# Kernel optimization log

Measured on AMD Instinct MI355X. Metric: run time of the kernel, lower is better.

The kernel has to match this reference:

```python
import jax, jax.numpy as jnp
import numpy as np

B, LQ, LP, D, H = 4, 512, 512, 512, 128


def setup_inputs() -> dict:
    key = jax.random.key(0)
    ks = jax.random.split(key, 5)
    hq = jax.random.normal(ks[0], (B, LQ, D), jnp.float32)
    hp = jax.random.normal(ks[1], (B, LP, D), jnp.float32)
    mask_hq = jnp.ones((B, LQ), dtype=bool)
    mask_hp = jnp.ones((B, LP), dtype=bool)
    # ln: Linear(2*D -> H) split into the hq / hp halves (algebraically identical
    # to concatenating then applying one Linear). Xavier-ish init scale.
    sc = 1.0 / np.sqrt(2 * D)
    Wq = jax.random.normal(ks[2], (D, H), jnp.float32) * sc
    Wp = jax.random.normal(ks[3], (D, H), jnp.float32) * sc
    b = jnp.zeros((H,), jnp.float32)
    v = jax.random.normal(ks[4], (H,), jnp.float32) / np.sqrt(H)
    return {"hq": hq, "hp": hp, "mask_hq": mask_hq, "mask_hp": mask_hp,
            "Wq": Wq, "Wp": Wp, "b": b, "v": v}


def reference(hq, hp, mask_hq, mask_hp, Wq, Wp, b, v):
    # ln(cat([hq_mat, hp_mat], -1)) == hq@Wq + hp@Wp + b  (decomposed, same math)
    pq = hq @ Wq                                  # (B, Lq, H)
    pp = hp @ Wp                                  # (B, Lp, H)
    h = jnp.tanh(pq[:, :, None, :] + pp[:, None, :, :] + b)   # (B, Lq, Lp, H)
    s = jnp.einsum('bqph,h->bqp', h, v)           # additive score (B, Lq, Lp)
    mask = mask_hq[:, :, None] & mask_hp[:, None, :]
    s = s - jnp.where(mask, 0.0, 10000.0).astype(s.dtype)
    a = jax.nn.softmax(s, axis=1)                 # softmax over Lq
    # q = sum_q a[b,q,p] * hq[b,q,:]  -> (B, Lp, D); dropout is identity (eval)
    return jnp.einsum('bqp,bqd->bpd', a, hq)
```

## Files before the change

### kernel.cpp

```cpp
#include <hip/hip_runtime.h>


#define NB 4
#define NLQ 512
#define NLP 512
#define ND 512
#define NH 128

#define KP 4
#define KSTRIDE ((size_t)2048 * NH)

#define SCL   2.8853900817779268f
#define LOG2E 1.4426950408889634f

typedef __attribute__((ext_vector_type(8))) short short8;
typedef __attribute__((ext_vector_type(4))) float f32x4;

__device__ __forceinline__ unsigned f2bf(float x) {
    unsigned u = __float_as_uint(x);
    return (u + 0x7FFFu + ((u >> 16) & 1u)) >> 16;
}
__device__ __forceinline__ float bf2f(unsigned h) { return __uint_as_float(h << 16); }

__global__ __launch_bounds__(256) void prep_kernel(
    const float* __restrict__ hq, const float* __restrict__ hp,
    const float* __restrict__ Wq, const float* __restrict__ Wp,
    unsigned short* __restrict__ Xh, unsigned short* __restrict__ Xl,
    unsigned short* __restrict__ WTh, unsigned short* __restrict__ WTl)
{
    __shared__ __align__(16) float wlds[128][132];
    const int bid = blockIdx.x, t = threadIdx.x;

    if (bid < 1024) {
        const int side = bid >> 9;
        const size_t base = (size_t)(bid & 511) * 2048 + (size_t)t * 8;
        const float* src = (side ? hp : hq) + base;
        float4 x0 = *reinterpret_cast<const float4*>(src);
        float4 x1 = *reinterpret_cast<const float4*>(src + 4);
        float v[8] = {x0.x,x0.y,x0.z,x0.w,x1.x,x1.y,x1.z,x1.w};
        unsigned uh[4], ul[4];
        #pragma unroll
        for (int j = 0; j < 4; ++j) {
            float a = v[2*j], c = v[2*j+1];
            unsigned ha = f2bf(a), hc = f2bf(c);
            unsigned la = f2bf(a - bf2f(ha)), lc = f2bf(c - bf2f(hc));
            uh[j] = ha | (hc << 16); ul[j] = la | (lc << 16);
        }
        unsigned short* dh = Xh + (size_t)side * 1048576 + base;
        unsigned short* dl = Xl + (size_t)side * 1048576 + base;
        *reinterpret_cast<uint4*>(dh) = make_uint4(uh[0],uh[1],uh[2],uh[3]);
        *reinterpret_cast<uint4*>(dl) = make_uint4(ul[0],ul[1],ul[2],ul[3]);
    } else {
        const int wb = bid - 1024;
        const int side = wb >> 2;
        const int k0 = (wb & 3) * 128;
        const float* W = side ? Wp : Wq;
        #pragma unroll
        for (int i = 0; i < 16; ++i) {
            int idx = t + i * 256;
            int r = idx >> 5, c4 = (idx & 31) * 4;
            *reinterpret_cast<float4*>(&wlds[r][c4]) =
                *reinterpret_cast<const float4*>(W + (size_t)(k0 + r) * NH + c4);
        }
        __syncthreads();
        const int h = t >> 1, seg = t & 1;
        unsigned short* dh = WTh + (size_t)side * 65536 + (size_t)h * 512 + k0 + seg * 64;
        unsigned short* dl = WTl + (size_t)side * 65536 + (size_t)h * 512 + k0 + seg * 64;
        for (int j = 0; j < 64; j += 4) {
            unsigned hh[4], ll[4];
            #pragma unroll
            for (int jj = 0; jj < 4; ++jj) {
                float w = wlds[seg * 64 + j + jj][h] * SCL;
                unsigned hb = f2bf(w);
                hh[jj] = hb; ll[jj] = f2bf(w - bf2f(hb));
            }
            *reinterpret_cast<uint2*>(dh + j) = make_uint2(hh[0]|(hh[1]<<16), hh[2]|(hh[3]<<16));
            *reinterpret_cast<uint2*>(dl + j) = make_uint2(ll[0]|(ll[1]<<16), ll[2]|(ll[3]<<16));
        }
    }
}

__global__ __launch_bounds__(256, 2) void proj_mfma_kernel(
    const unsigned short* __restrict__ Xh, const unsigned short* __restrict__ Xl,
    const unsigned short* __restrict__ WTh, const unsigned short* __restrict__ WTl,
    const float* __restrict__ bias,
    float* __restrict__ pqpart, float* __restrict__ pppart)
{
    __shared__ __align__(16) unsigned short XhL[32][40], XlL[32][40];
    __shared__ __align__(16) unsigned short WhL[128][40], WlL[128][40];

    const int row0 = blockIdx.x * 32;
    const int kk   = blockIdx.y;
    const int side = blockIdx.z;
    const int k0   = kk * 128;
    const int t = threadIdx.x;
    const int w = t >> 6, l = t & 63;
    const int rbase = 16 * (w & 1), hbase = 64 * (w >> 1);

    const unsigned short* xh = Xh + (size_t)side * 1048576;
    const unsigned short* xl = Xl + (size_t)side * 1048576;
    const unsigned short* wh = WTh + (size_t)side * 65536;
    const unsigned short* wl = WTl + (size_t)side * 65536;
    float* P = (side ? pppart : pqpart) + (size_t)kk * KSTRIDE;

    const int xr = t >> 3, xc = (t & 7) * 4;
    const int whh = t & 127, wseg = (t >> 7) * 16;

    f32x4 acc[4] = {};
    uint2 rxh, rxl; uint4 rwh0, rwh1, rwl0, rwl1;

    {   const size_t xo = (size_t)(row0 + xr) * 512 + k0 + xc;
        const size_t wo = (size_t)whh * 512 + k0 + wseg;
        rxh  = *reinterpret_cast<const uint2*>(xh + xo);
        rxl  = *reinterpret_cast<const uint2*>(xl + xo);
        rwh0 = *reinterpret_cast<const uint4*>(wh + wo);
        rwh1 = *reinterpret_cast<const uint4*>(wh + wo + 8);
        rwl0 = *reinterpret_cast<const uint4*>(wl + wo);
        rwl1 = *reinterpret_cast<const uint4*>(wl + wo + 8); }

    for (int st = 0; st < 4; ++st) {
        *reinterpret_cast<uint2*>(&XhL[xr][xc]) = rxh;
        *reinterpret_cast<uint2*>(&XlL[xr][xc]) = rxl;
        *reinterpret_cast<uint4*>(&WhL[whh][wseg])     = rwh0;
        *reinterpret_cast<uint4*>(&WhL[whh][wseg + 8]) = rwh1;
        *reinterpret_cast<uint4*>(&WlL[whh][wseg])     = rwl0;
        *reinterpret_cast<uint4*>(&WlL[whh][wseg + 8]) = rwl1;
        __syncthreads();
        if (st < 3) {
            const size_t xo = (size_t)(row0 + xr) * 512 + k0 + (st + 1) * 32 + xc;
            const size_t wo = (size_t)whh * 512 + k0 + (st + 1) * 32 + wseg;
            rxh  = *reinterpret_cast<const uint2*>(xh + xo);
            rxl  = *reinterpret_cast<const uint2*>(xl + xo);
            rwh0 = *reinterpret_cast<const uint4*>(wh + wo);
            rwh1 = *reinterpret_cast<const uint4*>(wh + wo + 8);
            rwl0 = *reinterpret_cast<const uint4*>(wl + wo);
            rwl1 = *reinterpret_cast<const uint4*>(wl + wo + 8);
        }
        short8 Ah = *reinterpret_cast<const short8*>(&XhL[rbase + (l & 15)][(l >> 4) * 8]);
        short8 Al = *reinterpret_cast<const short8*>(&XlL[rbase + (l & 15)][(l >> 4) * 8]);
        #pragma unroll
        for (int c = 0; c < 4; ++c) {
            short8 Bh = *reinterpret_cast<const short8*>(&WhL[hbase + c*16 + (l & 15)][(l >> 4) * 8]);
            short8 Bl = *reinterpret_cast<const short8*>(&WlL[hbase + c*16 + (l & 15)][(l >> 4) * 8]);
            acc[c] = __builtin_amdgcn_mfma_f32_16x16x32_bf16(Ah, Bh, acc[c], 0, 0, 0);
            acc[c] = __builtin_amdgcn_mfma_f32_16x16x32_bf16(Al, Bh, acc[c], 0, 0, 0);
            acc[c] = __builtin_amdgcn_mfma_f32_16x16x32_bf16(Ah, Bl, acc[c], 0, 0, 0);
        }
        __syncthreads();
    }

    const int orow = row0 + rbase + 4 * (l >> 4);
    #pragma unroll
    for (int c = 0; c < 4; ++c) {
        const int h = hbase + c * 16 + (l & 15);
        const float badd = (side == 0 && kk == 0) ? SCL * bias[h] : 0.f;
        #pragma unroll
        for (int i = 0; i < 4; ++i)
            P[(size_t)(orow + i) * NH + h] = acc[c][i] + badd;
    }
}

__global__ __launch_bounds__(256, 2) void scores_kernel(
    const float* __restrict__ pqpart,
    const float* __restrict__ pppart,
    const float* __restrict__ vvec,
    unsigned short* __restrict__ ebf,
    float* __restrict__ dsumpart)
{
    __shared__ float qT[NH][67];
    __shared__ float pT[NH][35];
    __shared__ __align__(16) float vL[NH];
    __shared__ float vsum_lds;

    const int qt = blockIdx.x * 64;
    const int pt = blockIdx.y * 32;
    const int b  = blockIdx.z;
    const int t  = threadIdx.x;

    {
        const float* src = pqpart + ((size_t)b * NLQ + qt) * NH;
        #pragma unroll
        for (int k = 0; k < 8; ++k) {
            int f4 = t + k * 256;
            int r = f4 >> 5, c = (f4 & 31) * 4;
            const float* p0 = src + (size_t)r * NH + c;
            float4 a  = *reinterpret_cast<const float4*>(p0);
            float4 b1 = *reinterpret_cast<const float4*>(p0 + KSTRIDE);
            float4 c1 = *reinterpret_cast<const float4*>(p0 + 2 * KSTRIDE);
            float4 d1 = *reinterpret_cast<const float4*>(p0 + 3 * KSTRIDE);
            qT[c + 0][r] = __builtin_amdgcn_exp2f(a.x + b1.x + c1.x + d1.x);
            qT[c + 1][r] = __builtin_amdgcn_exp2f(a.y + b1.y + c1.y + d1.y);
            qT[c + 2][r] = __builtin_amdgcn_exp2f(a.z + b1.z + c1.z + d1.z);
            qT[c + 3][r] = __builtin_amdgcn_exp2f(a.w + b1.w + c1.w + d1.w);
        }
        const float* src2 = pppart + ((size_t)b * NLP + pt) * NH;
        #pragma unroll
        for (int k = 0; k < 4; ++k) {
            int f4 = t + k * 256;
            int r = f4 >> 5, c = (f4 & 31) * 4;
            const float* p0 = src2 + (size_t)r * NH + c;
            float4 a  = *reinterpret_cast<const float4*>(p0);
            float4 b1 = *reinterpret_cast<const float4*>(p0 + KSTRIDE);
            float4 c1 = *reinterpret_cast<const float4*>(p0 + 2 * KSTRIDE);
            float4 d1 = *reinterpret_cast<const float4*>(p0 + 3 * KSTRIDE);
            pT[c + 0][r] = __builtin_amdgcn_exp2f(a.x + b1.x + c1.x + d1.x);
            pT[c + 1][r] = __builtin_amdgcn_exp2f(a.y + b1.y + c1.y + d1.y);
            pT[c + 2][r] = __builtin_amdgcn_exp2f(a.z + b1.z + c1.z + d1.z);
            pT[c + 3][r] = __builtin_amdgcn_exp2f(a.w + b1.w + c1.w + d1.w);
        }
        if (t < 32) *reinterpret_cast<float4*>(&vL[t * 4]) =
            *reinterpret_cast<const float4*>(vvec + t * 4);
    }
    __syncthreads();
    if (t < 64) {
        float s = vL[t] + vL[t + 64];
        #pragma unroll
        for (int off = 32; off; off >>= 1) s += __shfl_xor(s, off, 64);
        if (t == 0) vsum_lds = s * LOG2E;
    }
    __syncthreads();

    const int iq = t & 15;
    const int ip = t >> 4;

    float acc[4][2] = {};

    #pragma unroll 2
    for (int h = 0; h < NH; ++h) {
        float4 eq = *reinterpret_cast<const float4*>(&qT[h][4 * iq]);
        float2 ep = *reinterpret_cast<const float2*>(&pT[h][2 * ip]);
        float vh = vL[h];
        #pragma unroll
        for (int p = 0; p < 2; ++p) {
            float e  = p ? ep.y : ep.x;
            float za = fmaf(eq.x, e, 1.f), zb = fmaf(eq.y, e, 1.f);
            float zc = fmaf(eq.z, e, 1.f), zd = fmaf(eq.w, e, 1.f);
            float r1 = __builtin_amdgcn_rcpf(za * zb);
            float r2 = __builtin_amdgcn_rcpf(zc * zd);
            float v1 = vh * r1, v2 = vh * r2;
            acc[0][p] = fmaf(v1, zb, acc[0][p]);
            acc[1][p] = fmaf(v1, za, acc[1][p]);
            acc[2][p] = fmaf(v2, zd, acc[2][p]);
            acc[3][p] = fmaf(v2, zc, acc[3][p]);
        }
    }

    const float vs = vsum_lds;
    unsigned short* eo = ebf + ((size_t)b * NLP + pt + 2 * ip) * NLQ + qt + 4 * iq;
    float psum[2];
    #pragma unroll
    for (int p = 0; p < 2; ++p) {
        unsigned bb[4];
        float s = 0.f;
        #pragma unroll
        for (int j = 0; j < 4; ++j) {
            float e = __builtin_amdgcn_exp2f(fmaf(-SCL, acc[j][p], vs));
            bb[j] = f2bf(e);
            s += bf2f(bb[j]);
        }
        *reinterpret_cast<uint2*>(eo + (size_t)p * NLQ) =
            make_uint2(bb[0] | (bb[1] << 16), bb[2] | (bb[3] << 16));
        psum[p] = s;
    }
    #pragma unroll
    for (int off = 1; off < 16; off <<= 1) {
        psum[0] += __shfl_xor(psum[0], off, 64);
        psum[1] += __shfl_xor(psum[1], off, 64);
    }
    if ((t & 15) == 0) {
        dsumpart[((size_t)b * NLP + pt + 2 * ip + 0) * 8 + blockIdx.x] = psum[0];
        dsumpart[((size_t)b * NLP + pt + 2 * ip + 1) * 8 + blockIdx.x] = psum[1];
    }
}

__global__ __launch_bounds__(256, 2) void out_mfma_kernel(
    const unsigned short* __restrict__ ebf,
    const unsigned short* __restrict__ Xh,
    const unsigned short* __restrict__ Xl,
    const float* __restrict__ dsumpart,
    float* __restrict__ out)
{
    __shared__ __align__(16) unsigned short Ab[2][32][40];
    __shared__ __align__(16) unsigned short Hh[2][64][40];
    __shared__ __align__(16) unsigned short Hl[2][64][40];
    __shared__ float dsinv[32];

    const int pt = blockIdx.x;
    const int dt = blockIdx.y;
    const int bb = blockIdx.z;
    const int t  = threadIdx.x;
    const int w  = t >> 6, l = t & 63;
    const int poff = 16 * (w & 1), doff = 32 * (w >> 1);

    if (t < 32) {
        const float* dp = dsumpart + ((size_t)bb * NLP + pt * 32 + t) * 8;
        float s = 0.f;
        #pragma unroll
        for (int m = 0; m < 8; ++m) s += dp[m];
        dsinv[t] = 1.f / s;
    }

    const int ap = t >> 3, aq = (t & 7) * 4;
    const int hd = t & 63;
    const unsigned short* eb  = ebf + ((size_t)bb * NLP + pt * 32 + ap) * NLQ + aq;
    const unsigned short* hbh = Xh + ((size_t)bb * NLQ + 8 * w) * ND + dt * 64 + hd;
    const unsigned short* hbl = Xl + ((size_t)bb * NLQ + 8 * w) * ND + dt * 64 + hd;

    uint2 areg;
    unsigned shh[8], shl[8];

    areg = *reinterpret_cast<const uint2*>(eb);
    #pragma unroll
    for (int j = 0; j < 8; ++j) { shh[j] = hbh[(size_t)j * ND]; shl[j] = hbl[(size_t)j * ND]; }
    *reinterpret_cast<uint2*>(&Ab[0][ap][aq]) = areg;
    #pragma unroll
    for (int k = 0; k < 4; ++k) {
        *reinterpret_cast<unsigned*>(&Hh[0][hd][8*w + 2*k]) = shh[2*k] | (shh[2*k+1] << 16);
        *reinterpret_cast<unsigned*>(&Hl[0][hd][8*w + 2*k]) = shl[2*k] | (shl[2*k+1] << 16);
    }

    f32x4 acc0 = {0.f,0.f,0.f,0.f}, acc1 = {0.f,0.f,0.f,0.f};

    for (int st = 0; st < 16; ++st) {
        __syncthreads();
        const int cur = st & 1, nxt = cur ^ 1;
        if (st < 15) {
            areg = *reinterpret_cast<const uint2*>(eb + (st + 1) * 32);
            #pragma unroll
            for (int j = 0; j < 8; ++j) {
                shh[j] = hbh[((size_t)(st + 1) * 32 + j) * ND];
                shl[j] = hbl[((size_t)(st + 1) * 32 + j) * ND];
            }
        }
        short8 af  = *reinterpret_cast<const short8*>(&Ab[cur][poff + (l & 15)][(l >> 4) * 8]);
        short8 bh0 = *reinterpret_cast<const short8*>(&Hh[cur][doff +      (l & 15)][(l >> 4) * 8]);
        short8 bl0 = *reinterpret_cast<const short8*>(&Hl[cur][doff +      (l & 15)][(l >> 4) * 8]);
        short8 bh1 = *reinterpret_cast<const short8*>(&Hh[cur][doff + 16 + (l & 15)][(l >> 4) * 8]);
        short8 bl1 = *reinterpret_cast<const short8*>(&Hl[cur][doff + 16 + (l & 15)][(l >> 4) * 8]);
        acc0 = __builtin_amdgcn_mfma_f32_16x16x32_bf16(af, bh0, acc0, 0, 0, 0);
        acc0 = __builtin_amdgcn_mfma_f32_16x16x32_bf16(af, bl0, acc0, 0, 0, 0);
        acc1 = __builtin_amdgcn_mfma_f32_16x16x32_bf16(af, bh1, acc1, 0, 0, 0);
        acc1 = __builtin_amdgcn_mfma_f32_16x16x32_bf16(af, bl1, acc1, 0, 0, 0);
        if (st < 15) {
            *reinterpret_cast<uint2*>(&Ab[nxt][ap][aq]) = areg;
            #pragma unroll
            for (int k = 0; k < 4; ++k) {
                *reinterpret_cast<unsigned*>(&Hh[nxt][hd][8*w + 2*k]) = shh[2*k] | (shh[2*k+1] << 16);
                *reinterpret_cast<unsigned*>(&Hl[nxt][hd][8*w + 2*k]) = shl[2*k] | (shl[2*k+1] << 16);
            }
        }
    }

    const int orow = pt * 32 + poff + 4 * (l >> 4);
    const int ocol = dt * 64 + doff + (l & 15);
    float* ob = out + ((size_t)bb * NLP + orow) * ND + ocol;
    #pragma unroll
    for (int i = 0; i < 4; ++i) {
        float r = dsinv[poff + 4 * (l >> 4) + i];
        ob[(size_t)i * ND]      = acc0[i] * r;
        ob[(size_t)i * ND + 16] = acc1[i] * r;
    }
}

extern "C" void kernel_launch(void* const* d_in, const int* in_sizes, int n_in,
                              void* d_out, int out_size, void* d_ws, size_t ws_size,
                              hipStream_t stream) {
    const float* hq   = (const float*)d_in[0];
    const float* hp   = (const float*)d_in[1];
    const float* Wq   = (const float*)d_in[4];
    const float* Wp   = (const float*)d_in[5];
    const float* bias = (const float*)d_in[6];
    const float* vvec = (const float*)d_in[7];
    float* out = (float*)d_out;

    unsigned short* Xh  = (unsigned short*)d_ws;
    unsigned short* Xl  = Xh + 2097152;
    unsigned short* WTh = Xl + 2097152;
    unsigned short* WTl = WTh + 131072;
    float* pqpart = (float*)(WTl + 131072);
    float* pppart = pqpart + (size_t)KP * KSTRIDE;
    unsigned short* ebf = (unsigned short*)(pppart + (size_t)KP * KSTRIDE);
    float* dsumpart = (float*)(ebf + (size_t)NB * NLP * NLQ);

    prep_kernel<<<1032, 256, 0, stream>>>(hq, hp, Wq, Wp, Xh, Xl, WTh, WTl);
    proj_mfma_kernel<<<dim3(64, KP, 2), 256, 0, stream>>>(Xh, Xl, WTh, WTl, bias, pqpart, pppart);
    scores_kernel<<<dim3(8, 16, 4), 256, 0, stream>>>(pqpart, pppart, vvec, ebf, dsumpart);
    out_mfma_kernel<<<dim3(16, 8, 4), 256, 0, stream>>>(ebf, Xh, Xl, dsumpart, out);
}
```

Measured before the change: 56.64 us.

## Fuse bf16 split prep into projection kernel and shrink output tiles

Removes the separate prep kernel. The projection kernel now reads fp32 hq/hp and W directly, splits them into bf16 hi/lo in registers, and stages the whole 128-wide W slice in LDS. The hq side also writes out its split copy for the output GEMM, and hp is no longer materialized. The output kernel moves to 32-wide D tiles with twice the blocks and a higher occupancy hint, to raise parallelism. The trade-offs are a launch and a round trip saved against redundant W conversion in every block, larger LDS use, and strided global reads of W.

```diff
diff --git a/kernel.cpp b/kernel.cpp
--- a/kernel.cpp
+++ b/kernel.cpp
@@ -22,72 +22,15 @@
 }
 __device__ __forceinline__ float bf2f(unsigned h) { return __uint_as_float(h << 16); }
 
-__global__ __launch_bounds__(256) void prep_kernel(
+__global__ __launch_bounds__(256, 2) void proj_fused_kernel(
     const float* __restrict__ hq, const float* __restrict__ hp,
     const float* __restrict__ Wq, const float* __restrict__ Wp,
+    const float* __restrict__ bias,
     unsigned short* __restrict__ Xh, unsigned short* __restrict__ Xl,
-    unsigned short* __restrict__ WTh, unsigned short* __restrict__ WTl)
-{
-    __shared__ __align__(16) float wlds[128][132];
-    const int bid = blockIdx.x, t = threadIdx.x;
-
-    if (bid < 1024) {
-        const int side = bid >> 9;
-        const size_t base = (size_t)(bid & 511) * 2048 + (size_t)t * 8;
-        const float* src = (side ? hp : hq) + base;
-        float4 x0 = *reinterpret_cast<const float4*>(src);
-        float4 x1 = *reinterpret_cast<const float4*>(src + 4);
-        float v[8] = {x0.x,x0.y,x0.z,x0.w,x1.x,x1.y,x1.z,x1.w};
-        unsigned uh[4], ul[4];
-        #pragma unroll
-        for (int j = 0; j < 4; ++j) {
-            float a = v[2*j], c = v[2*j+1];
-            unsigned ha = f2bf(a), hc = f2bf(c);
-            unsigned la = f2bf(a - bf2f(ha)), lc = f2bf(c - bf2f(hc));
-            uh[j] = ha | (hc << 16); ul[j] = la | (lc << 16);
-        }
-        unsigned short* dh = Xh + (size_t)side * 1048576 + base;
-        unsigned short* dl = Xl + (size_t)side * 1048576 + base;
-        *reinterpret_cast<uint4*>(dh) = make_uint4(uh[0],uh[1],uh[2],uh[3]);
-        *reinterpret_cast<uint4*>(dl) = make_uint4(ul[0],ul[1],ul[2],ul[3]);
-    } else {
-        const int wb = bid - 1024;
-        const int side = wb >> 2;
-        const int k0 = (wb & 3) * 128;
-        const float* W = side ? Wp : Wq;
-        #pragma unroll
-        for (int i = 0; i < 16; ++i) {
-            int idx = t + i * 256;
-            int r = idx >> 5, c4 = (idx & 31) * 4;
-            *reinterpret_cast<float4*>(&wlds[r][c4]) =
-                *reinterpret_cast<const float4*>(W + (size_t)(k0 + r) * NH + c4);
-        }
-        __syncthreads();
-        const int h = t >> 1, seg = t & 1;
-        unsigned short* dh = WTh + (size_t)side * 65536 + (size_t)h * 512 + k0 + seg * 64;
-        unsigned short* dl = WTl + (size_t)side * 65536 + (size_t)h * 512 + k0 + seg * 64;
-        for (int j = 0; j < 64; j += 4) {
-            unsigned hh[4], ll[4];
-            #pragma unroll
-            for (int jj = 0; jj < 4; ++jj) {
-                float w = wlds[seg * 64 + j + jj][h] * SCL;
-                unsigned hb = f2bf(w);
-                hh[jj] = hb; ll[jj] = f2bf(w - bf2f(hb));
-            }
-            *reinterpret_cast<uint2*>(dh + j) = make_uint2(hh[0]|(hh[1]<<16), hh[2]|(hh[3]<<16));
-            *reinterpret_cast<uint2*>(dl + j) = make_uint2(ll[0]|(ll[1]<<16), ll[2]|(ll[3]<<16));
-        }
-    }
-}
-
-__global__ __launch_bounds__(256, 2) void proj_mfma_kernel(
-    const unsigned short* __restrict__ Xh, const unsigned short* __restrict__ Xl,
-    const unsigned short* __restrict__ WTh, const unsigned short* __restrict__ WTl,
-    const float* __restrict__ bias,
     float* __restrict__ pqpart, float* __restrict__ pppart)
 {
+    __shared__ __align__(16) unsigned short WhL[128][136], WlL[128][136];
     __shared__ __align__(16) unsigned short XhL[32][40], XlL[32][40];
-    __shared__ __align__(16) unsigned short WhL[128][40], WlL[128][40];
 
     const int row0 = blockIdx.x * 32;
     const int kk   = blockIdx.y;
@@ -97,51 +40,59 @@
     const int w = t >> 6, l = t & 63;
     const int rbase = 16 * (w & 1), hbase = 64 * (w >> 1);
 
-    const unsigned short* xh = Xh + (size_t)side * 1048576;
-    const unsigned short* xl = Xl + (size_t)side * 1048576;
-    const unsigned short* wh = WTh + (size_t)side * 65536;
-    const unsigned short* wl = WTl + (size_t)side * 65536;
+    const float* __restrict__ X = side ? hp : hq;
+    const float* __restrict__ W = side ? Wp : Wq;
     float* P = (side ? pppart : pqpart) + (size_t)kk * KSTRIDE;
 
+    {
+        const int h = t >> 1, seg = t & 1;
+        const float* wsrc = W + (size_t)(k0 + seg * 64) * NH + h;
+        for (int j = 0; j < 64; j += 4) {
+            unsigned hh[4], ll[4];
+            #pragma unroll
+            for (int jj = 0; jj < 4; ++jj) {
+                float wv = wsrc[(size_t)(j + jj) * NH] * SCL;
+                unsigned hb = f2bf(wv);
+                hh[jj] = hb; ll[jj] = f2bf(wv - bf2f(hb));
+            }
+            *reinterpret_cast<uint2*>(&WhL[h][seg * 64 + j]) =
+                make_uint2(hh[0] | (hh[1] << 16), hh[2] | (hh[3] << 16));
+            *reinterpret_cast<uint2*>(&WlL[h][seg * 64 + j]) =
+                make_uint2(ll[0] | (ll[1] << 16), ll[2] | (ll[3] << 16));
+        }
+    }
+
     const int xr = t >> 3, xc = (t & 7) * 4;
-    const int whh = t & 127, wseg = (t >> 7) * 16;
+    const float* xsrc = X + (size_t)(row0 + xr) * ND + k0 + xc;
 
     f32x4 acc[4] = {};
-    uint2 rxh, rxl; uint4 rwh0, rwh1, rwl0, rwl1;
-
-    {   const size_t xo = (size_t)(row0 + xr) * 512 + k0 + xc;
-        const size_t wo = (size_t)whh * 512 + k0 + wseg;
-        rxh  = *reinterpret_cast<const uint2*>(xh + xo);
-        rxl  = *reinterpret_cast<const uint2*>(xl + xo);
-        rwh0 = *reinterpret_cast<const uint4*>(wh + wo);
-        rwh1 = *reinterpret_cast<const uint4*>(wh + wo + 8);
-        rwl0 = *reinterpret_cast<const uint4*>(wl + wo);
-        rwl1 = *reinterpret_cast<const uint4*>(wl + wo + 8); }
+    float4 xreg = *reinterpret_cast<const float4*>(xsrc);
 
     for (int st = 0; st < 4; ++st) {
-        *reinterpret_cast<uint2*>(&XhL[xr][xc]) = rxh;
-        *reinterpret_cast<uint2*>(&XlL[xr][xc]) = rxl;
-        *reinterpret_cast<uint4*>(&WhL[whh][wseg])     = rwh0;
-        *reinterpret_cast<uint4*>(&WhL[whh][wseg + 8]) = rwh1;
-        *reinterpret_cast<uint4*>(&WlL[whh][wseg])     = rwl0;
-        *reinterpret_cast<uint4*>(&WlL[whh][wseg + 8]) = rwl1;
+        unsigned h0 = f2bf(xreg.x), h1 = f2bf(xreg.y);
+        unsigned h2 = f2bf(xreg.z), h3 = f2bf(xreg.w);
+        unsigned l0 = f2bf(xreg.x - bf2f(h0)), l1 = f2bf(xreg.y - bf2f(h1));
+        unsigned l2 = f2bf(xreg.z - bf2f(h2)), l3 = f2bf(xreg.w - bf2f(h3));
+        uint2 ph = make_uint2(h0 | (h1 << 16), h2 | (h3 << 16));
+        uint2 pl = make_uint2(l0 | (l1 << 16), l2 | (l3 << 16));
+        *reinterpret_cast<uint2*>(&XhL[xr][xc]) = ph;
+        *reinterpret_cast<uint2*>(&XlL[xr][xc]) = pl;
+        if (side == 0) {
+            const size_t po = (size_t)(row0 + xr) * ND + k0 + st * 32 + xc;
+            *reinterpret_cast<uint2*>(Xh + po) = ph;
+            *reinterpret_cast<uint2*>(Xl + po) = pl;
+        }
         __syncthreads();
-        if (st < 3) {
-            const size_t xo = (size_t)(row0 + xr) * 512 + k0 + (st + 1) * 32 + xc;
-            const size_t wo = (size_t)whh * 512 + k0 + (st + 1) * 32 + wseg;
-            rxh  = *reinterpret_cast<const uint2*>(xh + xo);
-            rxl  = *reinterpret_cast<const uint2*>(xl + xo);
-            rwh0 = *reinterpret_cast<const uint4*>(wh + wo);
-            rwh1 = *reinterpret_cast<const uint4*>(wh + wo + 8);
-            rwl0 = *reinterpret_cast<const uint4*>(wl + wo);
-            rwl1 = *reinterpret_cast<const uint4*>(wl + wo + 8);
-        }
+        if (st < 3) xreg = *reinterpret_cast<const float4*>(xsrc + (st + 1) * 32);
+
         short8 Ah = *reinterpret_cast<const short8*>(&XhL[rbase + (l & 15)][(l >> 4) * 8]);
         short8 Al = *reinterpret_cast<const short8*>(&XlL[rbase + (l & 15)][(l >> 4) * 8]);
         #pragma unroll
         for (int c = 0; c < 4; ++c) {
-            short8 Bh = *reinterpret_cast<const short8*>(&WhL[hbase + c*16 + (l & 15)][(l >> 4) * 8]);
-            short8 Bl = *reinterpret_cast<const short8*>(&WlL[hbase + c*16 + (l & 15)][(l >> 4) * 8]);
+            short8 Bh = *reinterpret_cast<const short8*>(
+                &WhL[hbase + c * 16 + (l & 15)][st * 32 + (l >> 4) * 8]);
+            short8 Bl = *reinterpret_cast<const short8*>(
+                &WlL[hbase + c * 16 + (l & 15)][st * 32 + (l >> 4) * 8]);
             acc[c] = __builtin_amdgcn_mfma_f32_16x16x32_bf16(Ah, Bh, acc[c], 0, 0, 0);
             acc[c] = __builtin_amdgcn_mfma_f32_16x16x32_bf16(Al, Bh, acc[c], 0, 0, 0);
             acc[c] = __builtin_amdgcn_mfma_f32_16x16x32_bf16(Ah, Bl, acc[c], 0, 0, 0);
@@ -273,7 +224,7 @@
     }
 }
 
-__global__ __launch_bounds__(256, 2) void out_mfma_kernel(
+__global__ __launch_bounds__(256, 4) void out_mfma_kernel(
     const unsigned short* __restrict__ ebf,
     const unsigned short* __restrict__ Xh,
     const unsigned short* __restrict__ Xl,
@@ -281,8 +232,8 @@
     float* __restrict__ out)
 {
     __shared__ __align__(16) unsigned short Ab[2][32][40];
-    __shared__ __align__(16) unsigned short Hh[2][64][40];
-    __shared__ __align__(16) unsigned short Hl[2][64][40];
+    __shared__ __align__(16) unsigned short Hh[2][32][40];
+    __shared__ __align__(16) unsigned short Hl[2][32][40];
     __shared__ float dsinv[32];
 
     const int pt = blockIdx.x;
@@ -290,7 +241,7 @@
     const int bb = blockIdx.z;
     const int t  = threadIdx.x;
     const int w  = t >> 6, l = t & 63;
-    const int poff = 16 * (w & 1), doff = 32 * (w >> 1);
+    const int poff = 16 * (w & 1), doff = 16 * (w >> 1);
 
     if (t < 32) {
         const float* dp = dsumpart + ((size_t)bb * NLP + pt * 32 + t) * 8;
@@ -301,25 +252,24 @@
     }
 
     const int ap = t >> 3, aq = (t & 7) * 4;
-    const int hd = t & 63;
+    const int hd = t & 31, qg = t >> 5;
     const unsigned short* eb  = ebf + ((size_t)bb * NLP + pt * 32 + ap) * NLQ + aq;
-    const unsigned short* hbh = Xh + ((size_t)bb * NLQ + 8 * w) * ND + dt * 64 + hd;
-    const unsigned short* hbl = Xl + ((size_t)bb * NLQ + 8 * w) * ND + dt * 64 + hd;
+    const unsigned short* hbh = Xh + ((size_t)bb * NLQ + qg * 4) * ND + dt * 32 + hd;
+    const unsigned short* hbl = Xl + ((size_t)bb * NLQ + qg * 4) * ND + dt * 32 + hd;
 
     uint2 areg;
-    unsigned shh[8], shl[8];
+    unsigned shh[4], shl[4];
 
     areg = *reinterpret_cast<const uint2*>(eb);
     #pragma unroll
-    for (int j = 0; j < 8; ++j) { shh[j] = hbh[(size_t)j * ND]; shl[j] = hbl[(size_t)j * ND]; }
+    for (int j = 0; j < 4; ++j) { shh[j] = hbh[(size_t)j * ND]; shl[j] = hbl[(size_t)j * ND]; }
     *reinterpret_cast<uint2*>(&Ab[0][ap][aq]) = areg;
-    #pragma unroll
-    for (int k = 0; k < 4; ++k) {
-        *reinterpret_cast<unsigned*>(&Hh[0][hd][8*w + 2*k]) = shh[2*k] | (shh[2*k+1] << 16);
-        *reinterpret_cast<unsigned*>(&Hl[0][hd][8*w + 2*k]) = shl[2*k] | (shl[2*k+1] << 16);
-    }
-
-    f32x4 acc0 = {0.f,0.f,0.f,0.f}, acc1 = {0.f,0.f,0.f,0.f};
+    *reinterpret_cast<unsigned*>(&Hh[0][hd][qg * 4])     = shh[0] | (shh[1] << 16);
+    *reinterpret_cast<unsigned*>(&Hh[0][hd][qg * 4 + 2]) = shh[2] | (shh[3] << 16);
+    *reinterpret_cast<unsigned*>(&Hl[0][hd][qg * 4])     = shl[0] | (shl[1] << 16);
+    *reinterpret_cast<unsigned*>(&Hl[0][hd][qg * 4 + 2]) = shl[2] | (shl[3] << 16);
+
+    f32x4 acc0 = {0.f,0.f,0.f,0.f};
 
     for (int st = 0; st < 16; ++st) {
         __syncthreads();
@@ -327,39 +277,31 @@
         if (st < 15) {
             areg = *reinterpret_cast<const uint2*>(eb + (st + 1) * 32);
             #pragma unroll
-            for (int j = 0; j < 8; ++j) {
+            for (int j = 0; j < 4; ++j) {
                 shh[j] = hbh[((size_t)(st + 1) * 32 + j) * ND];
                 shl[j] = hbl[((size_t)(st + 1) * 32 + j) * ND];
             }
         }
         short8 af  = *reinterpret_cast<const short8*>(&Ab[cur][poff + (l & 15)][(l >> 4) * 8]);
-        short8 bh0 = *reinterpret_cast<const short8*>(&Hh[cur][doff +      (l & 15)][(l >> 4) * 8]);
-        short8 bl0 = *reinterpret_cast<const short8*>(&Hl[cur][doff +      (l & 15)][(l >> 4) * 8]);
-        short8 bh1 = *reinterpret_cast<const short8*>(&Hh[cur][doff + 16 + (l & 15)][(l >> 4) * 8]);
-        short8 bl1 = *reinterpret_cast<const short8*>(&Hl[cur][doff + 16 + (l & 15)][(l >> 4) * 8]);
+        short8 bh0 = *reinterpret_cast<const short8*>(&Hh[cur][doff + (l & 15)][(l >> 4) * 8]);
+        short8 bl0 = *reinterpret_cast<const short8*>(&Hl[cur][doff + (l & 15)][(l >> 4) * 8]);
         acc0 = __builtin_amdgcn_mfma_f32_16x16x32_bf16(af, bh0, acc0, 0, 0, 0);
         acc0 = __builtin_amdgcn_mfma_f32_16x16x32_bf16(af, bl0, acc0, 0, 0, 0);
-        acc1 = __builtin_amdgcn_mfma_f32_16x16x32_bf16(af, bh1, acc1, 0, 0, 0);
-        acc1 = __builtin_amdgcn_mfma_f32_16x16x32_bf16(af, bl1, acc1, 0, 0, 0);
         if (st < 15) {
             *reinterpret_cast<uint2*>(&Ab[nxt][ap][aq]) = areg;
-            #pragma unroll
-            for (int k = 0; k < 4; ++k) {
-                *reinterpret_cast<unsigned*>(&Hh[nxt][hd][8*w + 2*k]) = shh[2*k] | (shh[2*k+1] << 16);
-                *reinterpret_cast<unsigned*>(&Hl[nxt][hd][8*w + 2*k]) = shl[2*k] | (shl[2*k+1] << 16);
-            }
+            *reinterpret_cast<unsigned*>(&Hh[nxt][hd][qg * 4])     = shh[0] | (shh[1] << 16);
+            *reinterpret_cast<unsigned*>(&Hh[nxt][hd][qg * 4 + 2]) = shh[2] | (shh[3] << 16);
+            *reinterpret_cast<unsigned*>(&Hl[nxt][hd][qg * 4])     = shl[0] | (shl[1] << 16);
+            *reinterpret_cast<unsigned*>(&Hl[nxt][hd][qg * 4 + 2]) = shl[2] | (shl[3] << 16);
         }
     }
 
     const int orow = pt * 32 + poff + 4 * (l >> 4);
-    const int ocol = dt * 64 + doff + (l & 15);
+    const int ocol = dt * 32 + doff + (l & 15);
     float* ob = out + ((size_t)bb * NLP + orow) * ND + ocol;
     #pragma unroll
-    for (int i = 0; i < 4; ++i) {
-        float r = dsinv[poff + 4 * (l >> 4) + i];
-        ob[(size_t)i * ND]      = acc0[i] * r;
-        ob[(size_t)i * ND + 16] = acc1[i] * r;
-    }
+    for (int i = 0; i < 4; ++i)
+        ob[(size_t)i * ND] = acc0[i] * dsinv[poff + 4 * (l >> 4) + i];
 }
 
 extern "C" void kernel_launch(void* const* d_in, const int* in_sizes, int n_in,
@@ -374,16 +316,14 @@
     float* out = (float*)d_out;
 
     unsigned short* Xh  = (unsigned short*)d_ws;
-    unsigned short* Xl  = Xh + 2097152;
-    unsigned short* WTh = Xl + 2097152;
-    unsigned short* WTl = WTh + 131072;
-    float* pqpart = (float*)(WTl + 131072);
+    unsigned short* Xl  = Xh + 1048576;
+    float* pqpart = (float*)(Xl + 1048576);
     float* pppart = pqpart + (size_t)KP * KSTRIDE;
     unsigned short* ebf = (unsigned short*)(pppart + (size_t)KP * KSTRIDE);
     float* dsumpart = (float*)(ebf + (size_t)NB * NLP * NLQ);
 
-    prep_kernel<<<1032, 256, 0, stream>>>(hq, hp, Wq, Wp, Xh, Xl, WTh, WTl);
-    proj_mfma_kernel<<<dim3(64, KP, 2), 256, 0, stream>>>(Xh, Xl, WTh, WTl, bias, pqpart, pppart);
+    proj_fused_kernel<<<dim3(64, KP, 2), 256, 0, stream>>>(hq, hp, Wq, Wp, bias,
+                                                           Xh, Xl, pqpart, pppart);
     scores_kernel<<<dim3(8, 16, 4), 256, 0, stream>>>(pqpart, pppart, vvec, ebf, dsumpart);
-    out_mfma_kernel<<<dim3(16, 8, 4), 256, 0, stream>>>(ebf, Xh, Xl, dsumpart, out);
-}
+    out_mfma_kernel<<<dim3(16, 16, 4), 256, 0, stream>>>(ebf, Xh, Xl, dsumpart, out);
+}
```

Result: faster. 53.13 us (-6.2%).
